# Kernel optimization log

Hardware: AMD Instinct MI355X
Metric: run time of the kernel (lower is better)

The kernel has to match this reference:

```python
import jax, jax.numpy as jnp
import numpy as np

B, T, D, H, UNITS = 32, 2048, 512, 512, 512

def setup_inputs() -> dict:
    key = jax.random.key(0)
    ks = jax.random.split(key, 5)
    scale = 0.02
    return {
        "features": jax.random.normal(ks[0], (B, T, D), dtype=jnp.float32),
        "hidden": jax.random.normal(ks[1], (B, H), dtype=jnp.float32),
        "Wk": jax.random.normal(ks[2], (D, UNITS), dtype=jnp.float32) * scale,
        "Wb": jnp.zeros((UNITS,), dtype=jnp.float32),
        "Uk": jax.random.normal(ks[3], (H, UNITS), dtype=jnp.float32) * scale,
        "Ub": jnp.zeros((UNITS,), dtype=jnp.float32),
        "Vk": jax.random.normal(ks[4], (UNITS, 1), dtype=jnp.float32) * scale,
        "Vb": jnp.zeros((1,), dtype=jnp.float32),
    }

def reference(features, hidden, Wk, Wb, Uk, Ub, Vk, Vb):
    # features: [B, T, D], hidden: [B, H]
    wf = jnp.einsum('btd,du->btu', features, Wk) + Wb          # [B, T, U]
    uh = (hidden @ Uk + Ub)[:, None, :]                        # [B, 1, U]
    score = jnp.tanh(wf + uh)                                  # [B, T, U]
    logits = jnp.einsum('btu,uo->bto', score, Vk) + Vb         # [B, T, 1]
    attention_weights = jax.nn.softmax(logits, axis=1)         # [B, T, 1]
    context_vector = jnp.sum(attention_weights * features, axis=1)  # [B, D]
    return context_vector, attention_weights
```

## Files before the change

kernel.cpp:

```cpp
#include <hip/hip_runtime.h>
#include <stdint.h>


typedef unsigned short ushort_t;
typedef __attribute__((ext_vector_type(8))) short short8;
typedef __attribute__((ext_vector_type(4))) float f32x4;
typedef __attribute__((ext_vector_type(2))) float float2v;
typedef __attribute__((ext_vector_type(2))) __bf16 bf162v;

__device__ __forceinline__ ushort_t f2bf(float f) {
    uint32_t u = __builtin_bit_cast(uint32_t, f);
    u = (u + 0x7fffu + ((u >> 16) & 1u)) >> 16;
    return (ushort_t)u;
}
__device__ __forceinline__ uint32_t pkbf(float a, float b) {
    bf162v r = __builtin_convertvector((float2v){a, b}, bf162v);
    return __builtin_bit_cast(uint32_t, r);
}

__global__ __launch_bounds__(256) void prep_all(
    const float* __restrict__ hidden, const float* __restrict__ Uk,
    const float* __restrict__ Ub, const float* __restrict__ Wb,
    const float* __restrict__ Wk,
    float* __restrict__ uh, ushort_t* __restrict__ WkTf)
{
    const int pb = blockIdx.x;
    if (pb < 256) {
        const int b  = pb >> 3;
        const int u  = (pb & 7) * 64 + (threadIdx.x & 63);
        const int k0 = (threadIdx.x >> 6) * 128;
        const float* hr = hidden + b * 512;
        float acc = 0.f;
        #pragma unroll 8
        for (int k = k0; k < k0 + 128; ++k)
            acc += hr[k] * Uk[k * 512 + u];
        __shared__ float red[256];
        red[threadIdx.x] = acc;
        __syncthreads();
        if (threadIdx.x < 64) {
            const int ul = threadIdx.x;
            uh[b * 512 + u] = red[ul] + red[ul + 64] + red[ul + 128] + red[ul + 192]
                            + Ub[u] + Wb[u];
        }
    } else {
        __shared__ float t[32][17];
        const int tid = threadIdx.x;
        #pragma unroll
        for (int e = 0; e < 2; ++e) {
            const int g  = (pb - 256) * 2 + e;
            const int ks = g >> 5;
            const int n4 = g & 31;
            #pragma unroll
            for (int q = 0; q < 2; ++q) {
                const int idx = q * 256 + tid;
                const int dl  = idx >> 4;
                const int ul  = idx & 15;
                t[dl][ul] = Wk[(size_t)(ks * 32 + dl) * 512 + n4 * 16 + ul];
            }
            __syncthreads();
            #pragma unroll
            for (int q = 0; q < 2; ++q) {
                const int idx  = q * 256 + tid;
                const int j    = idx & 7;
                const int lc   = (idx >> 3) & 15;
                const int quad = idx >> 7;
                WkTf[(size_t)g * 512 + idx] = f2bf(t[quad * 8 + j][lc]);
            }
            __syncthreads();
        }
    }
}

#define APAD 40
__global__ __launch_bounds__(512, 4) void attn_gemm(
    const float* __restrict__ feats, const ushort_t* __restrict__ WkTf,
    const float* __restrict__ uh, const float* __restrict__ Vk,
    float* __restrict__ lg)
{
    __shared__ __align__(16) short As[2][64 * APAD];
    __shared__ float uh_s[512];
    __shared__ float vk_s[512];
    __shared__ float lpart[8][64];

    const int tid  = threadIdx.x;
    const int lane = tid & 63;
    const int quad = lane >> 4;
    const int lc   = lane & 15;
    const int wn   = tid >> 6;
    const int m0   = blockIdx.x * 64;
    const int bidx = m0 >> 11;

    uh_s[tid] = uh[bidx * 512 + tid];
    vk_s[tid] = Vk[tid];

    const int rowA = tid >> 3;
    const int kAo  = (tid & 7) * 4;

    const ushort_t* bbase = WkTf + (size_t)(wn * 4) * 512 + quad * 128 + lc * 8;

    f32x4 acc[4][4];
    #pragma unroll
    for (int tm = 0; tm < 4; ++tm)
        #pragma unroll
        for (int tn = 0; tn < 4; ++tn)
            acc[tm][tn] = (f32x4){0.f, 0.f, 0.f, 0.f};

    {
        const f32x4 av = *(const f32x4*)(feats + (size_t)(m0 + rowA) * 512 + kAo);
        uint2 w;
        w.x = pkbf(av.x, av.y);
        w.y = pkbf(av.z, av.w);
        *(uint2*)(As[0] + rowA * APAD + kAo) = w;
    }

    int buf = 0;
    for (int ks = 0; ks < 16; ++ks) {
        __syncthreads();

        f32x4 a_next;
        const bool have = (ks + 1) < 16;
        if (have)
            a_next = *(const f32x4*)(feats + (size_t)(m0 + rowA) * 512
                                     + (ks + 1) * 32 + kAo);

        short8 af[4], bfr[4];
        const ushort_t* bk = bbase + (size_t)ks * 16384;
        #pragma unroll
        for (int t4 = 0; t4 < 4; ++t4)
            bfr[t4] = *(const short8*)(bk + t4 * 512);
        #pragma unroll
        for (int t4 = 0; t4 < 4; ++t4)
            af[t4] = *(const short8*)(As[buf] + (t4 * 16 + lc) * APAD + quad * 8);

        #pragma unroll
        for (int tm = 0; tm < 4; ++tm)
            #pragma unroll
            for (int tn = 0; tn < 4; ++tn)
                acc[tm][tn] = __builtin_amdgcn_mfma_f32_16x16x32_bf16(
                    af[tm], bfr[tn], acc[tm][tn], 0, 0, 0);

        if (have) {
            uint2 w;
            w.x = pkbf(a_next.x, a_next.y);
            w.y = pkbf(a_next.z, a_next.w);
            *(uint2*)(As[buf ^ 1] + rowA * APAD + kAo) = w;
        }
        buf ^= 1;
    }

    float rp[16];
    #pragma unroll
    for (int i = 0; i < 16; ++i) rp[i] = 0.f;
    #pragma unroll
    for (int tn = 0; tn < 4; ++tn) {
        const int nl  = wn * 64 + tn * 16 + lc;
        const float uhv = uh_s[nl];
        const float vkv = vk_s[nl];
        #pragma unroll
        for (int tm = 0; tm < 4; ++tm)
            #pragma unroll
            for (int i = 0; i < 4; ++i) {
                const float x = acc[tm][tn][i] + uhv;
                const float e = __expf(2.0f * x);
                rp[tm * 4 + i] += (1.0f - 2.0f / (e + 1.0f)) * vkv;
            }
    }
    #pragma unroll
    for (int i = 0; i < 16; ++i) {
        float v = rp[i];
        v += __shfl_xor(v, 1, 64);
        v += __shfl_xor(v, 2, 64);
        v += __shfl_xor(v, 4, 64);
        v += __shfl_xor(v, 8, 64);
        rp[i] = v;
    }
    if (lc == 0) {
        #pragma unroll
        for (int tm = 0; tm < 4; ++tm)
            #pragma unroll
            for (int i = 0; i < 4; ++i)
                lpart[wn][tm * 16 + quad * 4 + i] = rp[tm * 4 + i];
    }
    __syncthreads();
    if (tid < 64) {
        float s = 0.f;
        #pragma unroll
        for (int j = 0; j < 8; ++j) s += lpart[j][tid];
        lg[m0 + tid] = s;
    }
}

__global__ __launch_bounds__(256) void softmax_k(
    const float* __restrict__ lg, float* __restrict__ aw_out)
{
    const int b = blockIdx.x, tid = threadIdx.x;
    const float* p = lg + b * 2048;
    float v[8];
    #pragma unroll
    for (int i = 0; i < 8; ++i) v[i] = p[tid + i * 256];
    float mx = -1e30f;
    #pragma unroll
    for (int i = 0; i < 8; ++i) mx = fmaxf(mx, v[i]);
    #pragma unroll
    for (int off = 32; off >= 1; off >>= 1) mx = fmaxf(mx, __shfl_xor(mx, off, 64));
    __shared__ float redm[4], reds[4];
    const int wv = tid >> 6, ln = tid & 63;
    if (ln == 0) redm[wv] = mx;
    __syncthreads();
    mx = fmaxf(fmaxf(redm[0], redm[1]), fmaxf(redm[2], redm[3]));
    float s = 0.f;
    #pragma unroll
    for (int i = 0; i < 8; ++i) { v[i] = __expf(v[i] - mx); s += v[i]; }
    #pragma unroll
    for (int off = 32; off >= 1; off >>= 1) s += __shfl_xor(s, off, 64);
    if (ln == 0) reds[wv] = s;
    __syncthreads();
    s = reds[0] + reds[1] + reds[2] + reds[3];
    const float inv = 1.0f / s;
    #pragma unroll
    for (int i = 0; i < 8; ++i)
        aw_out[b * 2048 + tid + i * 256] = v[i] * inv;
}

__global__ __launch_bounds__(256) void context_part(
    const float* __restrict__ feats, const float* __restrict__ aw,
    float* __restrict__ part)
{
    const int b     = blockIdx.x >> 4;
    const int chunk = blockIdx.x & 15;
    const int half  = threadIdx.x >> 7;
    const int t0    = chunk * 128 + half * 64;
    const int d4    = (threadIdx.x & 127) * 4;
    const float* wp = aw + b * 2048 + t0;
    const float* fp = feats + (size_t)(b * 2048 + t0) * 512 + d4;
    f32x4 a = (f32x4){0.f, 0.f, 0.f, 0.f};
    #pragma unroll 4
    for (int tt = 0; tt < 64; ++tt) {
        const float w = wp[tt];
        const f32x4 f = *(const f32x4*)(fp + (size_t)tt * 512);
        a.x += w * f.x; a.y += w * f.y; a.z += w * f.z; a.w += w * f.w;
    }
    *(f32x4*)(part + (size_t)(b * 32 + chunk * 2 + half) * 512 + d4) = a;
}

__global__ __launch_bounds__(512) void context_reduce(
    const float* __restrict__ part, float* __restrict__ ctx)
{
    const int b = blockIdx.x;
    const int d = threadIdx.x;
    const float* p = part + (size_t)b * 32 * 512 + d;
    float s = 0.f;
    #pragma unroll
    for (int j = 0; j < 32; ++j) s += p[j * 512];
    ctx[b * 512 + d] = s;
}

extern "C" void kernel_launch(void* const* d_in, const int* in_sizes, int n_in,
                              void* d_out, int out_size, void* d_ws, size_t ws_size,
                              hipStream_t stream)
{
    const float* feats  = (const float*)d_in[0];
    const float* hidden = (const float*)d_in[1];
    const float* Wk     = (const float*)d_in[2];
    const float* Wb     = (const float*)d_in[3];
    const float* Uk     = (const float*)d_in[4];
    const float* Ub     = (const float*)d_in[5];
    const float* Vk     = (const float*)d_in[6];

    float* out       = (float*)d_out;
    float* ctx_out_p = out;
    float* aw_out_p  = out + 16384;

    char* ws = (char*)d_ws;
    float*    uh   = (float*)ws;
    ushort_t* WkTf = (ushort_t*)(ws + 65536);
    float*    lg   = (float*)(ws + 589824);
    float*    part = (float*)(ws + 851968);

    prep_all      <<<512, 256, 0, stream>>>(hidden, Uk, Ub, Wb, Wk, uh, WkTf);
    attn_gemm     <<<1024, 512, 0, stream>>>(feats, WkTf, uh, Vk, lg);
    softmax_k     <<<32,  256, 0, stream>>>(lg, aw_out_p);
    context_part  <<<512, 256, 0, stream>>>(feats, aw_out_p, part);
    context_reduce<<<32,  512, 0, stream>>>(part, ctx_out_p);
}
```

Baseline: 265.7 us.

## Load GEMM A fragments straight from global into registers, halve M tile

The attention GEMM no longer stages features through double-buffered LDS with block-wide barriers. Each wave now loads its bf16 A fragments directly from global memory into registers, converts them in place, and prefetches the next k-step of A and B into registers. The M tile per block drops from 64 to 32 rows and the grid doubles. This removes the LDS round-trip and the per-step __syncthreads, but all 8 waves now load the same feature rows redundantly, and B-fragment reuse per block is halved.

Measured after the change: 375.5 us. 41.3% more time.

```diff
diff --git a/kernel.cpp b/kernel.cpp
--- a/kernel.cpp
+++ b/kernel.cpp
@@ -5,6 +5,7 @@
 typedef unsigned short ushort_t;
 typedef __attribute__((ext_vector_type(8))) short short8;
 typedef __attribute__((ext_vector_type(4))) float f32x4;
+typedef __attribute__((ext_vector_type(4))) uint32_t u32x4;
 typedef __attribute__((ext_vector_type(2))) float float2v;
 typedef __attribute__((ext_vector_type(2))) __bf16 bf162v;
 
@@ -16,6 +17,11 @@
 __device__ __forceinline__ uint32_t pkbf(float a, float b) {
     bf162v r = __builtin_convertvector((float2v){a, b}, bf162v);
     return __builtin_bit_cast(uint32_t, r);
+}
+__device__ __forceinline__ short8 cvt8(const f32x4 lo, const f32x4 hi) {
+    u32x4 u = (u32x4){pkbf(lo.x, lo.y), pkbf(lo.z, lo.w),
+                      pkbf(hi.x, hi.y), pkbf(hi.z, hi.w)};
+    return __builtin_bit_cast(short8, u);
 }
 
 __global__ __launch_bounds__(256) void prep_all(
@@ -71,93 +77,84 @@
     }
 }
 
-#define APAD 40
 __global__ __launch_bounds__(512, 4) void attn_gemm(
     const float* __restrict__ feats, const ushort_t* __restrict__ WkTf,
     const float* __restrict__ uh, const float* __restrict__ Vk,
     float* __restrict__ lg)
 {
-    __shared__ __align__(16) short As[2][64 * APAD];
     __shared__ float uh_s[512];
     __shared__ float vk_s[512];
-    __shared__ float lpart[8][64];
+    __shared__ float lpart[8][32];
 
     const int tid  = threadIdx.x;
     const int lane = tid & 63;
     const int quad = lane >> 4;
     const int lc   = lane & 15;
     const int wn   = tid >> 6;
-    const int m0   = blockIdx.x * 64;
+    const int m0   = blockIdx.x * 32;
     const int bidx = m0 >> 11;
 
     uh_s[tid] = uh[bidx * 512 + tid];
     vk_s[tid] = Vk[tid];
 
-    const int rowA = tid >> 3;
-    const int kAo  = (tid & 7) * 4;
-
-    const ushort_t* bbase = WkTf + (size_t)(wn * 4) * 512 + quad * 128 + lc * 8;
-
-    f32x4 acc[4][4];
-    #pragma unroll
-    for (int tm = 0; tm < 4; ++tm)
+    const float* a_base0 = feats + (size_t)(m0 + lc) * 512 + quad * 8;
+    const float* a_base1 = feats + (size_t)(m0 + 16 + lc) * 512 + quad * 8;
+    const ushort_t* b_base = WkTf + (size_t)(wn * 4) * 512 + quad * 128 + lc * 8;
+
+    f32x4 acc[2][4];
+    #pragma unroll
+    for (int tm = 0; tm < 2; ++tm)
         #pragma unroll
         for (int tn = 0; tn < 4; ++tn)
             acc[tm][tn] = (f32x4){0.f, 0.f, 0.f, 0.f};
 
-    {
-        const f32x4 av = *(const f32x4*)(feats + (size_t)(m0 + rowA) * 512 + kAo);
-        uint2 w;
-        w.x = pkbf(av.x, av.y);
-        w.y = pkbf(av.z, av.w);
-        *(uint2*)(As[0] + rowA * APAD + kAo) = w;
-    }
-
-    int buf = 0;
+    f32x4 a[2][2][2];
+    short8 b[2][4];
+
+    a[0][0][0] = *(const f32x4*)(a_base0);
+    a[0][0][1] = *(const f32x4*)(a_base0 + 4);
+    a[0][1][0] = *(const f32x4*)(a_base1);
+    a[0][1][1] = *(const f32x4*)(a_base1 + 4);
+    #pragma unroll
+    for (int nf = 0; nf < 4; ++nf)
+        b[0][nf] = *(const short8*)(b_base + nf * 512);
+
+    #pragma unroll
     for (int ks = 0; ks < 16; ++ks) {
-        __syncthreads();
-
-        f32x4 a_next;
-        const bool have = (ks + 1) < 16;
-        if (have)
-            a_next = *(const f32x4*)(feats + (size_t)(m0 + rowA) * 512
-                                     + (ks + 1) * 32 + kAo);
-
-        short8 af[4], bfr[4];
-        const ushort_t* bk = bbase + (size_t)ks * 16384;
-        #pragma unroll
-        for (int t4 = 0; t4 < 4; ++t4)
-            bfr[t4] = *(const short8*)(bk + t4 * 512);
-        #pragma unroll
-        for (int t4 = 0; t4 < 4; ++t4)
-            af[t4] = *(const short8*)(As[buf] + (t4 * 16 + lc) * APAD + quad * 8);
-
-        #pragma unroll
-        for (int tm = 0; tm < 4; ++tm)
-            #pragma unroll
-            for (int tn = 0; tn < 4; ++tn)
-                acc[tm][tn] = __builtin_amdgcn_mfma_f32_16x16x32_bf16(
-                    af[tm], bfr[tn], acc[tm][tn], 0, 0, 0);
-
-        if (have) {
-            uint2 w;
-            w.x = pkbf(a_next.x, a_next.y);
-            w.y = pkbf(a_next.z, a_next.w);
-            *(uint2*)(As[buf ^ 1] + rowA * APAD + kAo) = w;
-        }
-        buf ^= 1;
-    }
-
-    float rp[16];
-    #pragma unroll
-    for (int i = 0; i < 16; ++i) rp[i] = 0.f;
+        const int cur = ks & 1;
+        const int nxt = cur ^ 1;
+        if (ks < 15) {
+            const int ko = (ks + 1) * 32;
+            a[nxt][0][0] = *(const f32x4*)(a_base0 + ko);
+            a[nxt][0][1] = *(const f32x4*)(a_base0 + ko + 4);
+            a[nxt][1][0] = *(const f32x4*)(a_base1 + ko);
+            a[nxt][1][1] = *(const f32x4*)(a_base1 + ko + 4);
+            const ushort_t* bk = b_base + (size_t)(ks + 1) * 16384;
+            #pragma unroll
+            for (int nf = 0; nf < 4; ++nf)
+                b[nxt][nf] = *(const short8*)(bk + nf * 512);
+        }
+        short8 af0 = cvt8(a[cur][0][0], a[cur][0][1]);
+        short8 af1 = cvt8(a[cur][1][0], a[cur][1][1]);
+        #pragma unroll
+        for (int tn = 0; tn < 4; ++tn) {
+            acc[0][tn] = __builtin_amdgcn_mfma_f32_16x16x32_bf16(
+                af0, b[cur][tn], acc[0][tn], 0, 0, 0);
+            acc[1][tn] = __builtin_amdgcn_mfma_f32_16x16x32_bf16(
+                af1, b[cur][tn], acc[1][tn], 0, 0, 0);
+        }
+    }
+
+    float rp[8];
+    #pragma unroll
+    for (int i = 0; i < 8; ++i) rp[i] = 0.f;
     #pragma unroll
     for (int tn = 0; tn < 4; ++tn) {
         const int nl  = wn * 64 + tn * 16 + lc;
         const float uhv = uh_s[nl];
         const float vkv = vk_s[nl];
         #pragma unroll
-        for (int tm = 0; tm < 4; ++tm)
+        for (int tm = 0; tm < 2; ++tm)
             #pragma unroll
             for (int i = 0; i < 4; ++i) {
                 const float x = acc[tm][tn][i] + uhv;
@@ -166,7 +163,7 @@
             }
     }
     #pragma unroll
-    for (int i = 0; i < 16; ++i) {
+    for (int i = 0; i < 8; ++i) {
         float v = rp[i];
         v += __shfl_xor(v, 1, 64);
         v += __shfl_xor(v, 2, 64);
@@ -176,13 +173,13 @@
     }
     if (lc == 0) {
         #pragma unroll
-        for (int tm = 0; tm < 4; ++tm)
+        for (int tm = 0; tm < 2; ++tm)
             #pragma unroll
             for (int i = 0; i < 4; ++i)
                 lpart[wn][tm * 16 + quad * 4 + i] = rp[tm * 4 + i];
     }
     __syncthreads();
-    if (tid < 64) {
+    if (tid < 32) {
         float s = 0.f;
         #pragma unroll
         for (int j = 0; j < 8; ++j) s += lpart[j][tid];
@@ -278,7 +275,7 @@
     float*    part = (float*)(ws + 851968);
 
     prep_all      <<<512, 256, 0, stream>>>(hidden, Uk, Ub, Wb, Wk, uh, WkTf);
-    attn_gemm     <<<1024, 512, 0, stream>>>(feats, WkTf, uh, Vk, lg);
+    attn_gemm     <<<2048, 512, 0, stream>>>(feats, WkTf, uh, Vk, lg);
     softmax_k     <<<32,  256, 0, stream>>>(lg, aw_out_p);
     context_part  <<<512, 256, 0, stream>>>(feats, aw_out_p, part);
     context_reduce<<<32,  512, 0, stream>>>(part, ctx_out_p);
```
